# Kernel tuning notes

Measured on AMD Instinct MI355X. Metric: run time of the kernel, lower is better.

Reference implementation:

```python
import jax, jax.numpy as jnp
import numpy as np
import math

NTOKEN, NINP, NHID, SEQ, BATCH = 33278, 400, 1150, 70, 16
ODE_STEPS = 8  # fixed-step RK4 over t in [0,1] (reference for the adaptive solver)


def lstm_layer(x, h0, c0, Wih, Whh, bih, bhh):
    # x: [S, B, in]; PyTorch gate order i, f, g, o
    def step(carry, xt):
        h, c = carry
        g = xt @ Wih.T + h @ Whh.T + bih + bhh
        i, f, gg, o = jnp.split(g, 4, axis=-1)
        c = jax.nn.sigmoid(f) * c + jax.nn.sigmoid(i) * jnp.tanh(gg)
        h = jax.nn.sigmoid(o) * jnp.tanh(c)
        return (h, c), h
    (hT, cT), ys = jax.lax.scan(step, (h0, c0), x)
    return ys, hT, cT


def cnf_delta_logp(E, cnf_W, cnf_b):
    # ODEnet: f(t,z) = relu(Linear(concat([t, z]))); exact divergence since
    # Jacobian diag = relu'(pre) * diag(Wx). Integrates dz/dt=f, d(dlogp)/dt=-div f.
    wt = cnf_W[:, 0]
    Wx = cnf_W[:, 1:]
    dWx = jnp.diag(Wx)

    def f(t, z):
        pre = z @ Wx.T + t * wt + cnf_b          # [ntoken, ninp]
        div = jnp.sum((pre > 0) * dWx, axis=-1)  # exact trace of df/dz
        return jax.nn.relu(pre), -div

    dt = 1.0 / ODE_STEPS

    def rk4(carry, t):
        z, dl = carry
        k1z, k1l = f(t, z)
        k2z, k2l = f(t + dt / 2, z + dt / 2 * k1z)
        k3z, k3l = f(t + dt / 2, z + dt / 2 * k2z)
        k4z, k4l = f(t + dt, z + dt * k3z)
        z = z + dt / 6 * (k1z + 2 * k2z + 2 * k3z + k4z)
        dl = dl + dt / 6 * (k1l + 2 * k2l + 2 * k3l + k4l)
        return (z, dl), None

    ts = jnp.arange(ODE_STEPS, dtype=E.dtype) * dt
    (zT, dl), _ = jax.lax.scan(rk4, (E, jnp.zeros(E.shape[0], E.dtype)), ts)
    return dl  # [ntoken]


def setup_inputs() -> dict:
    key = jax.random.key(0)
    ks = jax.random.split(key, 16)
    s = 0.1
    inp = {
        "tokens": jax.random.randint(ks[0], (SEQ, BATCH), 0, NTOKEN),
        "h0_0": jnp.zeros((BATCH, NHID), jnp.float32),
        "c0_0": jnp.zeros((BATCH, NHID), jnp.float32),
        "h0_1": jnp.zeros((BATCH, NHID), jnp.float32),
        "c0_1": jnp.zeros((BATCH, NHID), jnp.float32),
        "h0_2": jnp.zeros((BATCH, NINP), jnp.float32),
        "c0_2": jnp.zeros((BATCH, NINP), jnp.float32),
        "emb_W": jax.random.uniform(ks[1], (NTOKEN, NINP), jnp.float32, -s, s),
        "Wih0": jax.random.normal(ks[2], (4 * NHID, NINP), jnp.float32) * 0.02,
        "Whh0": jax.random.normal(ks[3], (4 * NHID, NHID), jnp.float32) * 0.02,
        "bih0": jnp.zeros((4 * NHID,), jnp.float32),
        "bhh0": jnp.zeros((4 * NHID,), jnp.float32),
        "Wih1": jax.random.normal(ks[4], (4 * NHID, NHID), jnp.float32) * 0.02,
        "Whh1": jax.random.normal(ks[5], (4 * NHID, NHID), jnp.float32) * 0.02,
        "bih1": jnp.zeros((4 * NHID,), jnp.float32),
        "bhh1": jnp.zeros((4 * NHID,), jnp.float32),
        "Wih2": jax.random.normal(ks[6], (4 * NINP, NHID), jnp.float32) * 0.02,
        "Whh2": jax.random.normal(ks[7], (4 * NINP, NINP), jnp.float32) * 0.02,
        "bih2": jnp.zeros((4 * NINP,), jnp.float32),
        "bhh2": jnp.zeros((4 * NINP,), jnp.float32),
        "cnf_W": jax.random.normal(ks[8], (NINP, NINP + 1), jnp.float32) * 0.05,
        "cnf_b": jnp.zeros((NINP,), jnp.float32),
    }
    return inp


def reference(tokens, h0_0, c0_0, h0_1, c0_1, h0_2, c0_2, emb_W,
              Wih0, Whh0, bih0, bhh0, Wih1, Whh1, bih1, bhh1,
              Wih2, Whh2, bih2, bhh2, cnf_W, cnf_b):
    # embedding (eval mode: all dropouts are identity)
    x = emb_W[tokens]                               # [S, B, ninp]
    x, h1, c1 = lstm_layer(x, h0_0, c0_0, Wih0, Whh0, bih0, bhh0)
    x, h2, c2 = lstm_layer(x, h0_1, c0_1, Wih1, Whh1, bih1, bhh1)
    x, h3, c3 = lstm_layer(x, h0_2, c0_2, Wih2, Whh2, bih2, bhh2)
    # nhidlast == ninp -> no latent projection
    h = x.reshape(SEQ * BATCH, NINP)

    # MVNLogProb vectorized: -0.5 ||E_v - h_i||^2 - k/2 log(2*pi)
    e2 = jnp.sum(emb_W * emb_W, axis=-1)            # [ntoken]
    h2n = jnp.sum(h * h, axis=-1, keepdims=True)    # [SB, 1]
    sq = e2[None, :] - 2.0 * (h @ emb_W.T) + h2n    # [SB, ntoken]
    log_pz0 = -0.5 * sq - (NINP / 2.0) * math.log(2.0 * math.pi)

    # CNF delta_logp is identical for every token position (loop-invariant)
    delta = cnf_delta_logp(emb_W, cnf_W, cnf_b)     # [ntoken]
    log_pz1 = log_pz0 - delta[None, :]

    prob = jax.nn.softmax(log_pz1, axis=-1)
    log_prob = jnp.log(prob + 1e-8)
    model_output = log_prob.reshape(SEQ, BATCH, NTOKEN)
    return model_output, h1, c1, h2, c2, h3, c3
```

## Files before the change

kernel.cpp:

```cpp
#include <hip/hip_runtime.h>
#include <hip/hip_bf16.h>
#include <math.h>

#define SEQL 70
#define NTOK 33278
#define ODE_STEPS 8
#define NBLK 242
#define NGRP 16
#define CZS 418

typedef __attribute__((ext_vector_type(4))) float f32x4;
typedef __attribute__((ext_vector_type(8))) short s16x8;
typedef unsigned short u16;

__device__ __forceinline__ u16 f2b(float f) {
    union { float f; unsigned int u; } a; a.f = f;
    unsigned int u = a.u;
    return (u16)((u + 0x7FFFu + ((u >> 16) & 1u)) >> 16);
}
__device__ __forceinline__ float b2f(u16 s) {
    union { unsigned int u; float f; } a; a.u = ((unsigned int)s) << 16;
    return a.f;
}

__device__ __forceinline__ unsigned czoff(int row, int colb) {
    unsigned s = ((colb < 768 ? (row & 7) : (row & 3)) << 4);
    return (unsigned)(row * 832 + (colb ^ (int)s));
}

__global__ void cvt_pad_k(const float* __restrict__ src, u16* __restrict__ dst,
                          int G, int Nin, int Nop, int Kin, int Kp, int rs, int co) {
    size_t total = (size_t)G * Nop * Kp;
    for (size_t idx = (size_t)blockIdx.x * 256 + threadIdx.x; idx < total;
         idx += (size_t)gridDim.x * 256) {
        int k = (int)(idx % Kp);
        size_t t2 = idx / Kp;
        int j = (int)(t2 % Nop);
        int g = (int)(t2 / Nop);
        float v = 0.f;
        if (j < Nin && k < Kin) v = src[((size_t)g * Nin + j) * rs + co + k];
        dst[idx] = f2b(v);
    }
}

__global__ void bias_k(const float* __restrict__ bih, const float* __restrict__ bhh,
                       float* __restrict__ o, int Nin, int Nop) {
    int idx = blockIdx.x * 256 + threadIdx.x;
    if (idx >= 4 * Nop) return;
    int g = idx / Nop, j = idx % Nop;
    o[idx] = (j < Nin) ? (bih[g * Nin + j] + bhh[g * Nin + j]) : 0.f;
}

__global__ void wtdwx_k(const float* __restrict__ cw, float* __restrict__ wt,
                        float* __restrict__ dwx) {
    int i = blockIdx.x * 256 + threadIdx.x;
    if (i < 400) {
        wt[i]  = cw[(size_t)i * 401];
        dwx[i] = cw[(size_t)i * 401 + 1 + i];
    }
}

__global__ void h0cvt_k(const float* __restrict__ h0, u16* __restrict__ hb, int N, int Kp) {
    int idx = blockIdx.x * 256 + threadIdx.x;
    if (idx >= 16 * Kp) return;
    int b = idx / Kp, k = idx % Kp;
    hb[idx] = f2b(k < N ? h0[b * N + k] : 0.f);
}

__global__ void embed_k(const int* __restrict__ tok, const float* __restrict__ emb,
                        u16* __restrict__ x0) {
    int idx = blockIdx.x * 256 + threadIdx.x;
    if (idx >= 1152 * 416) return;
    int r = idx / 416, k = idx - r * 416;
    float v = 0.f;
    if (r < SEQL * 16 && k < 400) v = emb[(size_t)tok[r] * 400 + k];
    x0[idx] = f2b(v);
}

__global__ void rowsumsq_k(const float* __restrict__ X, float* __restrict__ o, int K) {
    int r = blockIdx.x;
    const float* xr = X + (size_t)r * K;
    int lane = threadIdx.x;
    float s = 0.f;
    for (int k = lane; k < K; k += 64) { float v = xr[k]; s += v * v; }
#pragma unroll
    for (int off = 1; off < 64; off <<= 1) s += __shfl_xor(s, off, 64);
    if (lane == 0) o[r] = s;
}

__global__ void ucomb_k(const float* __restrict__ e2, const float* __restrict__ dl,
                        float* __restrict__ u) {
    int i = blockIdx.x * 256 + threadIdx.x;
    if (i < NTOK) u[i] = -0.5f * e2[i] - dl[i];
}

__global__ void gemm_bt_k(const u16* __restrict__ A, const u16* __restrict__ B,
                          float* __restrict__ C, int Kp, int lda, int ldb, int ldc,
                          int Mreal, int Nreal, const float* __restrict__ uvec) {
    const int tid = threadIdx.x;
    const int wid = tid >> 6, lane = tid & 63;
    const int la = lane & 15, lk = (lane >> 4) * 8;
    const int m0 = blockIdx.y * 64 + wid * 16;
    const int n0 = blockIdx.x * 64;
    const f32x4 Z4 = {0.f, 0.f, 0.f, 0.f};
    f32x4 acc[4] = {Z4, Z4, Z4, Z4};
    const u16* Ar = A + (size_t)(m0 + la) * lda + lk;
    const u16* Br = B + (size_t)(n0 + la) * ldb + lk;
    for (int k = 0; k < Kp; k += 32) {
        s16x8 a = *(const s16x8*)(Ar + k);
#pragma unroll
        for (int nt = 0; nt < 4; ++nt) {
            s16x8 b = *(const s16x8*)(Br + (size_t)nt * 16 * ldb + k);
            acc[nt] = __builtin_amdgcn_mfma_f32_16x16x32_bf16(a, b, acc[nt], 0, 0, 0);
        }
    }
    const int mr = m0 + (lane >> 4) * 4;
#pragma unroll
    for (int nt = 0; nt < 4; ++nt) {
        int cc = n0 + nt * 16 + la;
        if (cc >= Nreal) continue;
        float uv = uvec ? uvec[cc] : 0.f;
#pragma unroll
        for (int r = 0; r < 4; ++r) {
            int rr = mr + r;
            if (rr < Mreal) C[(size_t)rr * ldc + cc] = acc[nt][r] + uv;
        }
    }
}

__device__ __forceinline__ void gridbar(int* base, int nb, int iter) {
    __syncthreads();
    if (threadIdx.x == 0) {
        int grp = blockIdx.x & (NGRP - 1);
        int gsz = nb / NGRP + ((grp < (nb % NGRP)) ? 1 : 0);
        int* gc   = base + grp * 16;
        int* root = base + 256;
        int* gen  = base + 272;
        int old = __hip_atomic_fetch_add(gc, 1, __ATOMIC_ACQ_REL, __HIP_MEMORY_SCOPE_AGENT);
        if ((old % gsz) == gsz - 1) {
            int r = __hip_atomic_fetch_add(root, 1, __ATOMIC_ACQ_REL, __HIP_MEMORY_SCOPE_AGENT);
            if ((r % NGRP) == NGRP - 1)
                __hip_atomic_fetch_add(gen, 1, __ATOMIC_ACQ_REL, __HIP_MEMORY_SCOPE_AGENT);
        }
        while (__hip_atomic_load(gen, __ATOMIC_RELAXED, __HIP_MEMORY_SCOPE_AGENT) <= iter)
            __builtin_amdgcn_s_sleep(8);
        (void)__hip_atomic_load(gen, __ATOMIC_ACQUIRE, __HIP_MEMORY_SCOPE_AGENT);
    }
    __syncthreads();
}

__global__ __launch_bounds__(768, 3) void lstm_k(
    const float* __restrict__ c00, const float* __restrict__ c01,
    const float* __restrict__ c02,
    const u16* __restrict__ Whh0p, const u16* __restrict__ Wih1p,
    const u16* __restrict__ Whh1p, const u16* __restrict__ Wih2p,
    const u16* __restrict__ Whh2p,
    const float* __restrict__ xW0, const float* __restrict__ bias2v,
    const float* __restrict__ bias1v,
    u16* __restrict__ ys0s, u16* __restrict__ ys1s, u16* __restrict__ ys2s,
    float* __restrict__ oh1, float* __restrict__ oc1,
    float* __restrict__ oh2, float* __restrict__ oc2,
    float* __restrict__ oh3, float* __restrict__ oc3,
    int* __restrict__ bar)
{
    __shared__ __align__(16) char smem[162816];
    u16* wlds = (u16*)smem;
    float* gl = (float*)(smem + 147456);
    const int tid = threadIdx.x;
    const int bid = blockIdx.x;
    const int wv = tid >> 6, lane = tid & 63;
    const int la = lane & 15, lg = lane >> 4;

    int role, jb;
    if (bid < 72) { role = 0; jb = bid; }
    else if (bid < 216) { role = 1; jb = bid - 72; }
    else { role = 2; jb = bid - 216; }

    if (role == 0) {
        for (int s = tid; s < 4 * 36 * 64; s += 768) {
            int ln = s & 63, kt = (s >> 6) % 36, nt = s / (36 * 64);
            int row = nt * 1152 + jb * 16 + (ln & 15);
            int col = kt * 32 + (ln >> 4) * 8;
            *(s16x8*)(wlds + (size_t)s * 8) =
                *(const s16x8*)(Whh0p + (size_t)row * 1152 + col);
        }
    } else if (role == 1) {
        for (int s = tid; s < 2 * 72 * 64; s += 768) {
            int ln = s & 63, kt = (s >> 6) % 72, nt = s / (72 * 64);
            int lr = nt * 16 + (ln & 15);
            int row = (lr >> 3) * 1152 + jb * 8 + (lr & 7);
            int col8 = (ln >> 4) * 8;
            const u16* src = (kt < 36)
                ? Wih1p + (size_t)row * 1152 + kt * 32 + col8
                : Whh1p + (size_t)row * 1152 + (kt - 36) * 32 + col8;
            *(s16x8*)(wlds + (size_t)s * 8) = *(const s16x8*)src;
        }
    }
    __syncthreads();

    float c_reg = 0.f;
    for (int sg = 0; sg < 72; ++sg) {
        int t = sg - role;
        if (t >= 0 && t < SEQL) {
            f32x4 acc = {0.f, 0.f, 0.f, 0.f};
            if (role == 0) {
                int nt = wv / 3, kg = wv - nt * 3;
                const u16* ar = ys0s + ((size_t)sg * 16 + la) * 1152 + lg * 8;
                for (int kt = kg * 12; kt < kg * 12 + 12; ++kt) {
                    s16x8 a = *(const s16x8*)(ar + kt * 32);
                    s16x8 b = *(const s16x8*)(wlds + ((size_t)(nt * 36 + kt) * 64 + lane) * 8);
                    acc = __builtin_amdgcn_mfma_f32_16x16x32_bf16(a, b, acc, 0, 0, 0);
                }
                *(f32x4*)(gl + wv * 320 + la * 20 + lg * 4) = acc;
            } else if (role == 1) {
                int nt = wv / 6, kg = wv - nt * 6;
                const u16* ax = ys0s + ((size_t)sg * 16 + la) * 1152 + lg * 8;
                const u16* ah = ys1s + ((size_t)(sg - 1) * 16 + la) * 1152 + lg * 8;
                for (int kt = kg * 12; kt < kg * 12 + 12; ++kt) {
                    s16x8 a = (kt < 36) ? *(const s16x8*)(ax + kt * 32)
                                        : *(const s16x8*)(ah + (kt - 36) * 32);
                    s16x8 b = *(const s16x8*)(wlds + ((size_t)(nt * 72 + kt) * 64 + lane) * 8);
                    acc = __builtin_amdgcn_mfma_f32_16x16x32_bf16(a, b, acc, 0, 0, 0);
                }
                *(f32x4*)(gl + wv * 320 + la * 20 + lg * 4) = acc;
            } else {
                int nt = wv / 3, kg = wv - nt * 3;
                int k0 = (kg * 49) / 3, k1 = ((kg + 1) * 49) / 3;
                const u16* ax = ys1s + ((size_t)(sg - 1) * 16 + la) * 1152 + lg * 8;
                const u16* ah = ys2s + ((size_t)(sg - 2) * 16 + la) * 416 + lg * 8;
                int wr = nt * 416 + jb * 16 + la;
                for (int kt = k0; kt < k1; ++kt) {
                    s16x8 a, b;
                    if (kt < 36) {
                        a = *(const s16x8*)(ax + kt * 32);
                        b = *(const s16x8*)(Wih2p + (size_t)wr * 1152 + kt * 32 + lg * 8);
                    } else {
                        a = *(const s16x8*)(ah + (kt - 36) * 32);
                        b = *(const s16x8*)(Whh2p + (size_t)wr * 416 + (kt - 36) * 32 + lg * 8);
                    }
                    acc = __builtin_amdgcn_mfma_f32_16x16x32_bf16(a, b, acc, 0, 0, 0);
                }
                *(f32x4*)(gl + wv * 320 + la * 20 + lg * 4) = acc;
            }
            __syncthreads();
            if (role == 1) {
                if (tid < 128) {
                    int u = tid & 7, tb = tid >> 3;
                    int ug = jb * 8 + u;
                    float gv[4];
#pragma unroll
                    for (int g = 0; g < 4; ++g) {
                        int lr = g * 8 + u;
                        int nt = lr >> 4, li = lr & 15;
                        float s = 0.f;
#pragma unroll
                        for (int kg = 0; kg < 6; ++kg)
                            s += gl[(nt * 6 + kg) * 320 + li * 20 + tb];
                        gv[g] = s + bias1v[g * 1152 + ug];
                    }
                    float cprev = (t == 0) ? ((ug < 1150) ? c01[tb * 1150 + ug] : 0.f) : c_reg;
                    float si = 1.f / (1.f + expf(-gv[0]));
                    float sf = 1.f / (1.f + expf(-gv[1]));
                    float so = 1.f / (1.f + expf(-gv[3]));
                    float cn = sf * cprev + si * tanhf(gv[2]);
                    float hn = so * tanhf(cn);
                    c_reg = cn;
                    if (ug < 1150) {
                        ys1s[((size_t)sg * 16 + tb) * 1152 + ug] = f2b(hn);
                        if (t == SEQL - 1) { oh2[tb * 1150 + ug] = hn; oc2[tb * 1150 + ug] = cn; }
                    }
                }
            } else if (tid < 256) {
                int u = tid & 15, tb = tid >> 4;
                int ug = jb * 16 + u;
                float gv[4];
#pragma unroll
                for (int g = 0; g < 4; ++g) {
                    float s = 0.f;
#pragma unroll
                    for (int kg = 0; kg < 3; ++kg)
                        s += gl[(g * 3 + kg) * 320 + u * 20 + tb];
                    gv[g] = s + ((role == 0)
                                 ? xW0[((size_t)t * 16 + tb) * 4608 + g * 1152 + ug]
                                 : bias2v[g * 416 + ug]);
                }
                int N = (role == 0) ? 1150 : 400;
                const float* c0i = (role == 0) ? c00 : c02;
                float cprev = (t == 0) ? ((ug < N) ? c0i[tb * N + ug] : 0.f) : c_reg;
                float si = 1.f / (1.f + expf(-gv[0]));
                float sf = 1.f / (1.f + expf(-gv[1]));
                float so = 1.f / (1.f + expf(-gv[3]));
                float cn = sf * cprev + si * tanhf(gv[2]);
                float hn = so * tanhf(cn);
                c_reg = cn;
                if (ug < N) {
                    if (role == 0) {
                        ys0s[((size_t)(sg + 1) * 16 + tb) * 1152 + ug] = f2b(hn);
                        if (t == SEQL - 1) { oh1[tb * 1150 + ug] = hn; oc1[tb * 1150 + ug] = cn; }
                    } else {
                        ys2s[((size_t)(sg - 1) * 16 + tb) * 416 + ug] = f2b(hn);
                        if (t == SEQL - 1) { oh3[tb * 400 + ug] = hn; oc3[tb * 400 + ug] = cn; }
                    }
                }
            }
        }
        gridbar(bar, NBLK, sg);
    }
}

__global__ __launch_bounds__(512, 2) void cnf_k(const float* __restrict__ emb,
                                                const u16* __restrict__ Wxp,
                                                const float* __restrict__ wt,
                                                const float* __restrict__ bv,
                                                const float* __restrict__ dwx,
                                                float* __restrict__ dl) {
    __shared__ float z0s[64 * CZS];
    __shared__ __align__(16) u16 zi[64 * 416];
    const int tid = threadIdx.x;
    const int m0 = blockIdx.x * 64;

    for (int idx = tid; idx < 64 * 416; idx += 512) {
        int r = idx / 416, cc = idx - r * 416;
        int row = m0 + r;
        float v = (cc < 400 && row < NTOK) ? emb[(size_t)row * 400 + cc] : 0.f;
        if (cc < 416) z0s[r * CZS + cc] = v;
        *(u16*)((char*)zi + czoff(r, cc * 2)) = f2b(v);
    }

    const int wv = tid >> 6, lane = tid & 63;
    const int la = lane & 15, lg = lane >> 4;
    const int lk = lg * 8;
    const int Qw = (wv == 0) ? 4 : 3;
    const int ntb = (wv == 0) ? 0 : 4 + (wv - 1) * 3;

    float wtq[4], bq[4], dwq[4];
#pragma unroll
    for (int q = 0; q < 4; ++q) {
        if (q < Qw) {
            int col = (ntb + q) * 16 + la;
            wtq[q] = wt[col]; bq[q] = bv[col]; dwq[q] = dwx[col];
        } else { wtq[q] = 0.f; bq[q] = 0.f; dwq[q] = 0.f; }
    }
    __syncthreads();

    const float dt = 1.f / ODE_STEPS;
    const f32x4 Z4 = {0.f, 0.f, 0.f, 0.f};
    float Aacc[4][4][4];
#pragma unroll
    for (int m = 0; m < 4; ++m)
#pragma unroll
        for (int q = 0; q < 4; ++q)
#pragma unroll
            for (int r = 0; r < 4; ++r) Aacc[m][q][r] = 0.f;
    float divp[4][4];
#pragma unroll
    for (int m = 0; m < 4; ++m)
#pragma unroll
        for (int r = 0; r < 4; ++r) divp[m][r] = 0.f;

#pragma unroll 1
    for (int st = 0; st < ODE_STEPS; ++st) {
        float t0 = st * dt;
#pragma unroll 1
        for (int s = 0; s < 4; ++s) {
            float ts = t0 + ((s == 0) ? 0.f : (s == 3) ? dt : 0.5f * dt);
            float wgt = (s == 1 || s == 2) ? 2.f : 1.f;
            float cs = (s == 2) ? dt : 0.5f * dt;
            f32x4 pre[4][4];
#pragma unroll
            for (int m = 0; m < 4; ++m)
#pragma unroll
                for (int q = 0; q < 4; ++q) pre[m][q] = Z4;
#pragma unroll 1
            for (int kk = 0; kk < 13; ++kk) {
                s16x8 b[4];
#pragma unroll
                for (int q = 0; q < 4; ++q)
                    if (q < Qw)
                        b[q] = *(const s16x8*)(Wxp + (size_t)((ntb + q) * 16 + la) * 416 +
                                               kk * 32 + lk);
#pragma unroll
                for (int m = 0; m < 4; ++m) {
                    int row = m * 16 + la;
                    s16x8 a = *(const s16x8*)((const char*)zi + czoff(row, (kk * 64 + lg * 16)));
#pragma unroll
                    for (int q = 0; q < 4; ++q)
                        if (q < Qw)
                            pre[m][q] = __builtin_amdgcn_mfma_f32_16x16x32_bf16(
                                a, b[q], pre[m][q], 0, 0, 0);
                }
            }
            __syncthreads();
#pragma unroll
            for (int m = 0; m < 4; ++m) {
#pragma unroll
                for (int q = 0; q < 4; ++q) {
                    if (q >= Qw) continue;
                    int col = (ntb + q) * 16 + la;
#pragma unroll
                    for (int r = 0; r < 4; ++r) {
                        int row = m * 16 + lg * 4 + r;
                        float pv = pre[m][q][r] + ts * wtq[q] + bq[q];
                        float kz = fmaxf(pv, 0.f);
                        if (pv > 0.f) divp[m][r] += dwq[q] * wgt;
                        float An = Aacc[m][q][r] + wgt * kz;
                        float ev;
                        if (s < 3) {
                            Aacc[m][q][r] = An;
                            ev = z0s[row * CZS + col] + cs * kz;
                        } else {
                            float zn = z0s[row * CZS + col] + (dt / 6.f) * An;
                            z0s[row * CZS + col] = zn;
                            Aacc[m][q][r] = 0.f;
                            ev = zn;
                        }
                        *(u16*)((char*)zi + czoff(row, col * 2)) = f2b(ev);
                    }
                }
            }
            __syncthreads();
        }
    }

#pragma unroll
    for (int m = 0; m < 4; ++m)
#pragma unroll
        for (int r = 0; r < 4; ++r) {
            float v = divp[m][r];
            v += __shfl_xor(v, 1, 64);
            v += __shfl_xor(v, 2, 64);
            v += __shfl_xor(v, 4, 64);
            v += __shfl_xor(v, 8, 64);
            divp[m][r] = v;
        }
    float* dsc = (float*)zi;
    if (la == 0) {
#pragma unroll
        for (int m = 0; m < 4; ++m)
#pragma unroll
            for (int r = 0; r < 4; ++r)
                dsc[wv * 64 + m * 16 + lg * 4 + r] = divp[m][r];
    }
    __syncthreads();
    for (int row = tid; row < 64; row += 512) {
        float s = 0.f;
#pragma unroll
        for (int w = 0; w < 8; ++w) s += dsc[w * 64 + row];
        if (m0 + row < NTOK) dl[m0 + row] = -(dt / 6.f) * s;
    }
}

__global__ void logsoftmax_k(float* __restrict__ L, int n) {
    const int row = blockIdx.x;
    float* R = L + (size_t)row * n;
    const int tid = threadIdx.x;
    float mx = -INFINITY, s = 0.f;
    for (int c = tid; c < n; c += 256) {
        float v = R[c];
        float nm = fmaxf(mx, v);
        s = s * expf(mx - nm) + expf(v - nm);
        mx = nm;
    }
#pragma unroll
    for (int off = 1; off < 64; off <<= 1) {
        float om = __shfl_xor(mx, off, 64);
        float os = __shfl_xor(s, off, 64);
        float nm = fmaxf(mx, om);
        s = s * expf(mx - nm) + os * expf(om - nm);
        mx = nm;
    }
    __shared__ float smx[4], ssm[4];
    if ((tid & 63) == 0) { smx[tid >> 6] = mx; ssm[tid >> 6] = s; }
    __syncthreads();
    float bm = fmaxf(fmaxf(smx[0], smx[1]), fmaxf(smx[2], smx[3]));
    float bs = ssm[0] * expf(smx[0] - bm) + ssm[1] * expf(smx[1] - bm) +
               ssm[2] * expf(smx[2] - bm) + ssm[3] * expf(smx[3] - bm);
    float lz = logf(bs);
    for (int c = tid; c < n; c += 256) {
        float v = R[c];
        R[c] = logf(expf(v - bm) + 1e-8f * bs) - lz;
    }
}

extern "C" void kernel_launch(void* const* d_in, const int* in_sizes, int n_in,
                              void* d_out, int out_size, void* d_ws, size_t ws_size,
                              hipStream_t stream) {
    const int*   tokens = (const int*)d_in[0];
    const float* h00 = (const float*)d_in[1];
    const float* c00 = (const float*)d_in[2];
    const float* h01 = (const float*)d_in[3];
    const float* c01 = (const float*)d_in[4];
    const float* h02 = (const float*)d_in[5];
    const float* c02 = (const float*)d_in[6];
    const float* embW = (const float*)d_in[7];
    const float* Wih0 = (const float*)d_in[8];
    const float* Whh0 = (const float*)d_in[9];
    const float* bih0 = (const float*)d_in[10];
    const float* bhh0 = (const float*)d_in[11];
    const float* Wih1 = (const float*)d_in[12];
    const float* Whh1 = (const float*)d_in[13];
    const float* bih1 = (const float*)d_in[14];
    const float* bhh1 = (const float*)d_in[15];
    const float* Wih2 = (const float*)d_in[16];
    const float* Whh2 = (const float*)d_in[17];
    const float* bih2 = (const float*)d_in[18];
    const float* bhh2 = (const float*)d_in[19];
    const float* cnfW = (const float*)d_in[20];
    const float* cnfb = (const float*)d_in[21];
    float* out = (float*)d_out;

    char* p = (char*)d_ws;
    auto alloc = [&](size_t bytes) -> void* {
        void* r = (void*)p;
        p += (bytes + 255) & ~(size_t)255;
        return r;
    };
    u16*   emb_p = (u16*)alloc((size_t)33280 * 416 * 2);
    u16*   x0    = (u16*)alloc((size_t)1152 * 416 * 2);
    u16*   ys0s  = (u16*)alloc((size_t)1136 * 1152 * 2);
    u16*   ys1s  = (u16*)alloc((size_t)1136 * 1152 * 2);
    u16*   ys2s  = (u16*)alloc((size_t)1184 * 416 * 2);
    float* xW    = (float*)alloc((size_t)1120 * 4608 * 4);
    u16*   Wih0p = (u16*)alloc((size_t)4608 * 416 * 2);
    u16*   Whh0p = (u16*)alloc((size_t)4608 * 1152 * 2);
    u16*   Wih1p = (u16*)alloc((size_t)4608 * 1152 * 2);
    u16*   Whh1p = (u16*)alloc((size_t)4608 * 1152 * 2);
    u16*   Wih2p = (u16*)alloc((size_t)1664 * 1152 * 2);
    u16*   Whh2p = (u16*)alloc((size_t)1664 * 416 * 2);
    float* bias0 = (float*)alloc((size_t)4608 * 4);
    float* bias1 = (float*)alloc((size_t)4608 * 4);
    float* bias2 = (float*)alloc((size_t)1664 * 4);
    u16*   Wxp   = (u16*)alloc((size_t)416 * 416 * 2);
    float* wtv   = (float*)alloc((size_t)400 * 4);
    float* dwx   = (float*)alloc((size_t)400 * 4);
    float* dl    = (float*)alloc((size_t)NTOK * 4);
    float* e2    = (float*)alloc((size_t)NTOK * 4);
    float* uvec  = (float*)alloc((size_t)NTOK * 4);
    int*   bar   = (int*)alloc(4096);

    size_t OM = (size_t)SEQL * 16 * NTOK;
    float* oh1 = out + OM;
    float* oc1 = oh1 + 16 * 1150;
    float* oh2 = oc1 + 16 * 1150;
    float* oc2 = oh2 + 16 * 1150;
    float* oh3 = oc2 + 16 * 1150;
    float* oc3 = oh3 + 16 * 400;

    hipMemsetAsync(bar, 0, 4096, stream);
    hipMemsetAsync(ys0s, 0, (size_t)1136 * 1152 * 2, stream);
    hipMemsetAsync(ys1s, 0, (size_t)1136 * 1152 * 2, stream);
    hipMemsetAsync(ys2s, 0, (size_t)1184 * 416 * 2, stream);

    cvt_pad_k<<<2048, 256, 0, stream>>>(Wih0, Wih0p, 4, 1150, 1152, 400, 416, 400, 0);
    cvt_pad_k<<<2048, 256, 0, stream>>>(Whh0, Whh0p, 4, 1150, 1152, 1150, 1152, 1150, 0);
    cvt_pad_k<<<2048, 256, 0, stream>>>(Wih1, Wih1p, 4, 1150, 1152, 1150, 1152, 1150, 0);
    cvt_pad_k<<<2048, 256, 0, stream>>>(Whh1, Whh1p, 4, 1150, 1152, 1150, 1152, 1150, 0);
    cvt_pad_k<<<2048, 256, 0, stream>>>(Wih2, Wih2p, 4, 400, 416, 1150, 1152, 1150, 0);
    cvt_pad_k<<<2048, 256, 0, stream>>>(Whh2, Whh2p, 4, 400, 416, 400, 416, 400, 0);
    cvt_pad_k<<<2048, 256, 0, stream>>>(embW, emb_p, 1, 33278, 33280, 400, 416, 400, 0);
    cvt_pad_k<<<2048, 256, 0, stream>>>(cnfW, Wxp, 1, 400, 416, 400, 416, 401, 1);
    bias_k<<<(4 * 1152 + 255) / 256, 256, 0, stream>>>(bih0, bhh0, bias0, 1150, 1152);
    bias_k<<<(4 * 1152 + 255) / 256, 256, 0, stream>>>(bih1, bhh1, bias1, 1150, 1152);
    bias_k<<<(4 * 416 + 255) / 256, 256, 0, stream>>>(bih2, bhh2, bias2, 400, 416);
    wtdwx_k<<<2, 256, 0, stream>>>(cnfW, wtv, dwx);
    rowsumsq_k<<<NTOK, 64, 0, stream>>>(embW, e2, 400);

    h0cvt_k<<<(16 * 1152 + 255) / 256, 256, 0, stream>>>(h00, ys0s, 1150, 1152);
    h0cvt_k<<<(16 * 1152 + 255) / 256, 256, 0, stream>>>(h01, ys1s, 1150, 1152);
    h0cvt_k<<<(16 * 416 + 255) / 256, 256, 0, stream>>>(h02, ys2s, 400, 416);

    cnf_k<<<520, 512, 0, stream>>>(embW, Wxp, wtv, cnfb, dwx, dl);
    ucomb_k<<<(NTOK + 255) / 256, 256, 0, stream>>>(e2, dl, uvec);

    embed_k<<<(1152 * 416 + 255) / 256, 256, 0, stream>>>(tokens, embW, x0);
    gemm_bt_k<<<dim3(72, 18), 256, 0, stream>>>(x0, Wih0p, xW, 416, 416, 416, 4608,
                                                1120, 4608, bias0);

    lstm_k<<<NBLK, 768, 0, stream>>>(
        c00, c01, c02, Whh0p, Wih1p, Whh1p, Wih2p, Whh2p,
        xW, bias2, bias1, ys0s, ys1s, ys2s,
        oh1, oc1, oh2, oc2, oh3, oc3, bar);

    gemm_bt_k<<<dim3(520, 18), 256, 0, stream>>>(ys2s + (size_t)16 * 416, emb_p, out,
                                                 416, 416, 416, NTOK, 1120, NTOK, uvec);
    logsoftmax_k<<<1120, 256, 0, stream>>>(out, NTOK);
}
```

Before: 2.998 ms.

## Replace global grid barrier with per-role barriers and restructure CNF kernel

The persistent LSTM kernel drops the single grid-wide barrier per skewed step. Each layer role now syncs only among its own blocks and waits on a generation counter published by the upstream layer. This lets layers run ahead as a dataflow pipeline instead of in lockstep. The CNF kernel also moves to 768 threads with 12 waves, swaps the MFMA operands so each lane holds 4 contiguous columns, and does vectorized z/weight loads and packed bf16 stores. The risks are correctness of the new barrier and counter layout, and higher register and LDS pressure in the CNF kernel.

```diff
diff --git a/kernel.cpp b/kernel.cpp
--- a/kernel.cpp
+++ b/kernel.cpp
@@ -6,8 +6,7 @@
 #define NTOK 33278
 #define ODE_STEPS 8
 #define NBLK 242
-#define NGRP 16
-#define CZS 418
+#define CZ4 404
 
 typedef __attribute__((ext_vector_type(4))) float f32x4;
 typedef __attribute__((ext_vector_type(8))) short s16x8;
@@ -128,22 +127,30 @@
     }
 }
 
-__device__ __forceinline__ void gridbar(int* base, int nb, int iter) {
+__device__ __forceinline__ void rolebar(int* base, int nb, int ngrp, int roleBlk, int iter) {
     __syncthreads();
     if (threadIdx.x == 0) {
-        int grp = blockIdx.x & (NGRP - 1);
-        int gsz = nb / NGRP + ((grp < (nb % NGRP)) ? 1 : 0);
+        int grp = roleBlk % ngrp;
+        int gsz = nb / ngrp + ((grp < (nb % ngrp)) ? 1 : 0);
         int* gc   = base + grp * 16;
-        int* root = base + 256;
-        int* gen  = base + 272;
+        int* root = base + ngrp * 16;
+        int* gen  = base + ngrp * 16 + 16;
         int old = __hip_atomic_fetch_add(gc, 1, __ATOMIC_ACQ_REL, __HIP_MEMORY_SCOPE_AGENT);
         if ((old % gsz) == gsz - 1) {
             int r = __hip_atomic_fetch_add(root, 1, __ATOMIC_ACQ_REL, __HIP_MEMORY_SCOPE_AGENT);
-            if ((r % NGRP) == NGRP - 1)
+            if ((r % ngrp) == ngrp - 1)
                 __hip_atomic_fetch_add(gen, 1, __ATOMIC_ACQ_REL, __HIP_MEMORY_SCOPE_AGENT);
         }
         while (__hip_atomic_load(gen, __ATOMIC_RELAXED, __HIP_MEMORY_SCOPE_AGENT) <= iter)
-            __builtin_amdgcn_s_sleep(8);
+            __builtin_amdgcn_s_sleep(4);
+        (void)__hip_atomic_load(gen, __ATOMIC_ACQUIRE, __HIP_MEMORY_SCOPE_AGENT);
+    }
+    __syncthreads();
+}
+__device__ __forceinline__ void waitgen(int* gen, int needed) {
+    if (threadIdx.x == 0) {
+        while (__hip_atomic_load(gen, __ATOMIC_RELAXED, __HIP_MEMORY_SCOPE_AGENT) < needed)
+            __builtin_amdgcn_s_sleep(4);
         (void)__hip_atomic_load(gen, __ATOMIC_ACQUIRE, __HIP_MEMORY_SCOPE_AGENT);
     }
     __syncthreads();
@@ -176,6 +183,12 @@
     else if (bid < 216) { role = 1; jb = bid - 72; }
     else { role = 2; jb = bid - 216; }
 
+    int* bar0 = bar;
+    int* bar1 = bar + 256;
+    int* bar2 = bar + 768;
+    int* g0 = bar0 + 144;
+    int* g1 = bar1 + 272;
+
     if (role == 0) {
         for (int s = tid; s < 4 * 36 * 64; s += 768) {
             int ln = s & 63, kt = (s >> 6) % 36, nt = s / (36 * 64);
@@ -199,164 +212,163 @@
     __syncthreads();
 
     float c_reg = 0.f;
-    for (int sg = 0; sg < 72; ++sg) {
-        int t = sg - role;
-        if (t >= 0 && t < SEQL) {
-            f32x4 acc = {0.f, 0.f, 0.f, 0.f};
-            if (role == 0) {
-                int nt = wv / 3, kg = wv - nt * 3;
-                const u16* ar = ys0s + ((size_t)sg * 16 + la) * 1152 + lg * 8;
-                for (int kt = kg * 12; kt < kg * 12 + 12; ++kt) {
-                    s16x8 a = *(const s16x8*)(ar + kt * 32);
-                    s16x8 b = *(const s16x8*)(wlds + ((size_t)(nt * 36 + kt) * 64 + lane) * 8);
-                    acc = __builtin_amdgcn_mfma_f32_16x16x32_bf16(a, b, acc, 0, 0, 0);
+    for (int t = 0; t < SEQL; ++t) {
+        if (role == 1) waitgen(g0, t + 1);
+        else if (role == 2) waitgen(g1, t + 1);
+
+        f32x4 acc = {0.f, 0.f, 0.f, 0.f};
+        if (role == 0) {
+            int nt = wv / 3, kg = wv - nt * 3;
+            const u16* ar = ys0s + ((size_t)t * 16 + la) * 1152 + lg * 8;
+            for (int kt = kg * 12; kt < kg * 12 + 12; ++kt) {
+                s16x8 a = *(const s16x8*)(ar + kt * 32);
+                s16x8 b = *(const s16x8*)(wlds + ((size_t)(nt * 36 + kt) * 64 + lane) * 8);
+                acc = __builtin_amdgcn_mfma_f32_16x16x32_bf16(a, b, acc, 0, 0, 0);
+            }
+            *(f32x4*)(gl + wv * 320 + la * 20 + lg * 4) = acc;
+        } else if (role == 1) {
+            int nt = wv / 6, kg = wv - nt * 6;
+            const u16* ax = ys0s + ((size_t)(t + 1) * 16 + la) * 1152 + lg * 8;
+            const u16* ah = ys1s + ((size_t)t * 16 + la) * 1152 + lg * 8;
+            for (int kt = kg * 12; kt < kg * 12 + 12; ++kt) {
+                s16x8 a = (kt < 36) ? *(const s16x8*)(ax + kt * 32)
+                                    : *(const s16x8*)(ah + (kt - 36) * 32);
+                s16x8 b = *(const s16x8*)(wlds + ((size_t)(nt * 72 + kt) * 64 + lane) * 8);
+                acc = __builtin_amdgcn_mfma_f32_16x16x32_bf16(a, b, acc, 0, 0, 0);
+            }
+            *(f32x4*)(gl + wv * 320 + la * 20 + lg * 4) = acc;
+        } else {
+            int nt = wv / 3, kg = wv - nt * 3;
+            int k0 = (kg * 49) / 3, k1 = ((kg + 1) * 49) / 3;
+            const u16* ax = ys1s + ((size_t)(t + 1) * 16 + la) * 1152 + lg * 8;
+            const u16* ah = ys2s + ((size_t)t * 16 + la) * 416 + lg * 8;
+            int wr = nt * 416 + jb * 16 + la;
+            for (int kt = k0; kt < k1; ++kt) {
+                s16x8 a, b;
+                if (kt < 36) {
+                    a = *(const s16x8*)(ax + kt * 32);
+                    b = *(const s16x8*)(Wih2p + (size_t)wr * 1152 + kt * 32 + lg * 8);
+                } else {
+                    a = *(const s16x8*)(ah + (kt - 36) * 32);
+                    b = *(const s16x8*)(Whh2p + (size_t)wr * 416 + (kt - 36) * 32 + lg * 8);
                 }
-                *(f32x4*)(gl + wv * 320 + la * 20 + lg * 4) = acc;
-            } else if (role == 1) {
-                int nt = wv / 6, kg = wv - nt * 6;
-                const u16* ax = ys0s + ((size_t)sg * 16 + la) * 1152 + lg * 8;
-                const u16* ah = ys1s + ((size_t)(sg - 1) * 16 + la) * 1152 + lg * 8;
-                for (int kt = kg * 12; kt < kg * 12 + 12; ++kt) {
-                    s16x8 a = (kt < 36) ? *(const s16x8*)(ax + kt * 32)
-                                        : *(const s16x8*)(ah + (kt - 36) * 32);
-                    s16x8 b = *(const s16x8*)(wlds + ((size_t)(nt * 72 + kt) * 64 + lane) * 8);
-                    acc = __builtin_amdgcn_mfma_f32_16x16x32_bf16(a, b, acc, 0, 0, 0);
+                acc = __builtin_amdgcn_mfma_f32_16x16x32_bf16(a, b, acc, 0, 0, 0);
+            }
+            *(f32x4*)(gl + wv * 320 + la * 20 + lg * 4) = acc;
+        }
+        __syncthreads();
+        if (role == 1) {
+            if (tid < 128) {
+                int u = tid & 7, tb = tid >> 3;
+                int ug = jb * 8 + u;
+                float gv[4];
+#pragma unroll
+                for (int g = 0; g < 4; ++g) {
+                    int lr = g * 8 + u;
+                    int nt = lr >> 4, li = lr & 15;
+                    float s = 0.f;
+#pragma unroll
+                    for (int kg = 0; kg < 6; ++kg)
+                        s += gl[(nt * 6 + kg) * 320 + li * 20 + tb];
+                    gv[g] = s + bias1v[g * 1152 + ug];
                 }
-                *(f32x4*)(gl + wv * 320 + la * 20 + lg * 4) = acc;
-            } else {
-                int nt = wv / 3, kg = wv - nt * 3;
-                int k0 = (kg * 49) / 3, k1 = ((kg + 1) * 49) / 3;
-                const u16* ax = ys1s + ((size_t)(sg - 1) * 16 + la) * 1152 + lg * 8;
-                const u16* ah = ys2s + ((size_t)(sg - 2) * 16 + la) * 416 + lg * 8;
-                int wr = nt * 416 + jb * 16 + la;
-                for (int kt = k0; kt < k1; ++kt) {
-                    s16x8 a, b;
-                    if (kt < 36) {
-                        a = *(const s16x8*)(ax + kt * 32);
-                        b = *(const s16x8*)(Wih2p + (size_t)wr * 1152 + kt * 32 + lg * 8);
-                    } else {
-                        a = *(const s16x8*)(ah + (kt - 36) * 32);
-                        b = *(const s16x8*)(Whh2p + (size_t)wr * 416 + (kt - 36) * 32 + lg * 8);
-                    }
-                    acc = __builtin_amdgcn_mfma_f32_16x16x32_bf16(a, b, acc, 0, 0, 0);
-                }
-                *(f32x4*)(gl + wv * 320 + la * 20 + lg * 4) = acc;
-            }
-            __syncthreads();
-            if (role == 1) {
-                if (tid < 128) {
-                    int u = tid & 7, tb = tid >> 3;
-                    int ug = jb * 8 + u;
-                    float gv[4];
-#pragma unroll
-                    for (int g = 0; g < 4; ++g) {
-                        int lr = g * 8 + u;
-                        int nt = lr >> 4, li = lr & 15;
-                        float s = 0.f;
-#pragma unroll
-                        for (int kg = 0; kg < 6; ++kg)
-                            s += gl[(nt * 6 + kg) * 320 + li * 20 + tb];
-                        gv[g] = s + bias1v[g * 1152 + ug];
-                    }
-                    float cprev = (t == 0) ? ((ug < 1150) ? c01[tb * 1150 + ug] : 0.f) : c_reg;
-                    float si = 1.f / (1.f + expf(-gv[0]));
-                    float sf = 1.f / (1.f + expf(-gv[1]));
-                    float so = 1.f / (1.f + expf(-gv[3]));
-                    float cn = sf * cprev + si * tanhf(gv[2]);
-                    float hn = so * tanhf(cn);
-                    c_reg = cn;
-                    if (ug < 1150) {
-                        ys1s[((size_t)sg * 16 + tb) * 1152 + ug] = f2b(hn);
-                        if (t == SEQL - 1) { oh2[tb * 1150 + ug] = hn; oc2[tb * 1150 + ug] = cn; }
-                    }
-                }
-            } else if (tid < 256) {
-                int u = tid & 15, tb = tid >> 4;
-                int ug = jb * 16 + u;
-                float gv[4];
-#pragma unroll
-                for (int g = 0; g < 4; ++g) {
-                    float s = 0.f;
-#pragma unroll
-                    for (int kg = 0; kg < 3; ++kg)
-                        s += gl[(g * 3 + kg) * 320 + u * 20 + tb];
-                    gv[g] = s + ((role == 0)
-                                 ? xW0[((size_t)t * 16 + tb) * 4608 + g * 1152 + ug]
-                                 : bias2v[g * 416 + ug]);
-                }
-                int N = (role == 0) ? 1150 : 400;
-                const float* c0i = (role == 0) ? c00 : c02;
-                float cprev = (t == 0) ? ((ug < N) ? c0i[tb * N + ug] : 0.f) : c_reg;
+                float cprev = (t == 0) ? ((ug < 1150) ? c01[tb * 1150 + ug] : 0.f) : c_reg;
                 float si = 1.f / (1.f + expf(-gv[0]));
                 float sf = 1.f / (1.f + expf(-gv[1]));
                 float so = 1.f / (1.f + expf(-gv[3]));
                 float cn = sf * cprev + si * tanhf(gv[2]);
                 float hn = so * tanhf(cn);
                 c_reg = cn;
-                if (ug < N) {
-                    if (role == 0) {
-                        ys0s[((size_t)(sg + 1) * 16 + tb) * 1152 + ug] = f2b(hn);
-                        if (t == SEQL - 1) { oh1[tb * 1150 + ug] = hn; oc1[tb * 1150 + ug] = cn; }
-                    } else {
-                        ys2s[((size_t)(sg - 1) * 16 + tb) * 416 + ug] = f2b(hn);
-                        if (t == SEQL - 1) { oh3[tb * 400 + ug] = hn; oc3[tb * 400 + ug] = cn; }
-                    }
+                if (ug < 1150) {
+                    ys1s[((size_t)(t + 1) * 16 + tb) * 1152 + ug] = f2b(hn);
+                    if (t == SEQL - 1) { oh2[tb * 1150 + ug] = hn; oc2[tb * 1150 + ug] = cn; }
                 }
             }
-        }
-        gridbar(bar, NBLK, sg);
-    }
-}
-
-__global__ __launch_bounds__(512, 2) void cnf_k(const float* __restrict__ emb,
+        } else if (tid < 256) {
+            int u = tid & 15, tb = tid >> 4;
+            int ug = jb * 16 + u;
+            float gv[4];
+#pragma unroll
+            for (int g = 0; g < 4; ++g) {
+                float s = 0.f;
+#pragma unroll
+                for (int kg = 0; kg < 3; ++kg)
+                    s += gl[(g * 3 + kg) * 320 + u * 20 + tb];
+                gv[g] = s + ((role == 0)
+                             ? xW0[((size_t)t * 16 + tb) * 4608 + g * 1152 + ug]
+                             : bias2v[g * 416 + ug]);
+            }
+            int N = (role == 0) ? 1150 : 400;
+            const float* c0i = (role == 0) ? c00 : c02;
+            float cprev = (t == 0) ? ((ug < N) ? c0i[tb * N + ug] : 0.f) : c_reg;
+            float si = 1.f / (1.f + expf(-gv[0]));
+            float sf = 1.f / (1.f + expf(-gv[1]));
+            float so = 1.f / (1.f + expf(-gv[3]));
+            float cn = sf * cprev + si * tanhf(gv[2]);
+            float hn = so * tanhf(cn);
+            c_reg = cn;
+            if (ug < N) {
+                if (role == 0) {
+                    ys0s[((size_t)(t + 1) * 16 + tb) * 1152 + ug] = f2b(hn);
+                    if (t == SEQL - 1) { oh1[tb * 1150 + ug] = hn; oc1[tb * 1150 + ug] = cn; }
+                } else {
+                    ys2s[((size_t)(t + 1) * 16 + tb) * 416 + ug] = f2b(hn);
+                    if (t == SEQL - 1) { oh3[tb * 400 + ug] = hn; oc3[tb * 400 + ug] = cn; }
+                }
+            }
+        }
+        if (role == 0) rolebar(bar0, 72, 8, jb, t);
+        else if (role == 1) rolebar(bar1, 144, 16, jb, t);
+        else rolebar(bar2, 26, 1, jb, t);
+    }
+}
+
+__global__ __launch_bounds__(768, 3) void cnf_k(const float* __restrict__ emb,
                                                 const u16* __restrict__ Wxp,
-                                                const float* __restrict__ wt,
-                                                const float* __restrict__ bv,
-                                                const float* __restrict__ dwx,
+                                                const float* __restrict__ wtv,
+                                                const float* __restrict__ bvv,
+                                                const float* __restrict__ dwxv,
                                                 float* __restrict__ dl) {
-    __shared__ float z0s[64 * CZS];
-    __shared__ __align__(16) u16 zi[64 * 416];
+    __shared__ __align__(16) char smem[159744];
+    float* z0s = (float*)smem;
+    char*  zib = smem + 64 * CZ4 * 4;
+    float* dsc = (float*)(smem + 64 * CZ4 * 4 + 64 * 832);
     const int tid = threadIdx.x;
     const int m0 = blockIdx.x * 64;
-
-    for (int idx = tid; idx < 64 * 416; idx += 512) {
+    const int wv = tid >> 6, lane = tid & 63;
+    const int la = lane & 15, lg = lane >> 4;
+
+    for (int idx = tid; idx < 64 * 416; idx += 768) {
         int r = idx / 416, cc = idx - r * 416;
         int row = m0 + r;
         float v = (cc < 400 && row < NTOK) ? emb[(size_t)row * 400 + cc] : 0.f;
-        if (cc < 416) z0s[r * CZS + cc] = v;
-        *(u16*)((char*)zi + czoff(r, cc * 2)) = f2b(v);
-    }
-
-    const int wv = tid >> 6, lane = tid & 63;
-    const int la = lane & 15, lg = lane >> 4;
-    const int lk = lg * 8;
-    const int Qw = (wv == 0) ? 4 : 3;
-    const int ntb = (wv == 0) ? 0 : 4 + (wv - 1) * 3;
-
-    float wtq[4], bq[4], dwq[4];
-#pragma unroll
-    for (int q = 0; q < 4; ++q) {
+        if (cc < 400) z0s[r * CZ4 + cc] = v;
+        *(u16*)(zib + czoff(r, cc * 2)) = f2b(v);
+    }
+
+    const int Qw = (wv == 0) ? 3 : 2;
+    const int ntb = (wv == 0) ? 0 : 3 + 2 * (wv - 1);
+    const f32x4 Z4 = {0.f, 0.f, 0.f, 0.f};
+    f32x4 wt4[3], bv4[3], dw4[3];
+#pragma unroll
+    for (int q = 0; q < 3; ++q) {
+        wt4[q] = Z4; bv4[q] = Z4; dw4[q] = Z4;
         if (q < Qw) {
-            int col = (ntb + q) * 16 + la;
-            wtq[q] = wt[col]; bq[q] = bv[col]; dwq[q] = dwx[col];
-        } else { wtq[q] = 0.f; bq[q] = 0.f; dwq[q] = 0.f; }
-    }
-    __syncthreads();
-
-    const float dt = 1.f / ODE_STEPS;
-    const f32x4 Z4 = {0.f, 0.f, 0.f, 0.f};
-    float Aacc[4][4][4];
+            int c4 = (ntb + q) * 16 + lg * 4;
+            wt4[q] = *(const f32x4*)(wtv + c4);
+            bv4[q] = *(const f32x4*)(bvv + c4);
+            dw4[q] = *(const f32x4*)(dwxv + c4);
+        }
+    }
+    __syncthreads();
+
+    const float dt = 1.f / ODE_STEPS, dt6 = dt / 6.f;
+    f32x4 Aacc[4][3];
 #pragma unroll
     for (int m = 0; m < 4; ++m)
 #pragma unroll
-        for (int q = 0; q < 4; ++q)
-#pragma unroll
-            for (int r = 0; r < 4; ++r) Aacc[m][q][r] = 0.f;
-    float divp[4][4];
-#pragma unroll
-    for (int m = 0; m < 4; ++m)
-#pragma unroll
-        for (int r = 0; r < 4; ++r) divp[m][r] = 0.f;
+        for (int q = 0; q < 3; ++q) Aacc[m][q] = Z4;
+    float divacc[4] = {0.f, 0.f, 0.f, 0.f};
 
 #pragma unroll 1
     for (int st = 0; st < ODE_STEPS; ++st) {
@@ -366,87 +378,79 @@
             float ts = t0 + ((s == 0) ? 0.f : (s == 3) ? dt : 0.5f * dt);
             float wgt = (s == 1 || s == 2) ? 2.f : 1.f;
             float cs = (s == 2) ? dt : 0.5f * dt;
-            f32x4 pre[4][4];
+            f32x4 pre[4][3];
 #pragma unroll
             for (int m = 0; m < 4; ++m)
 #pragma unroll
-                for (int q = 0; q < 4; ++q) pre[m][q] = Z4;
-#pragma unroll 1
+                for (int q = 0; q < 3; ++q) pre[m][q] = Z4;
             for (int kk = 0; kk < 13; ++kk) {
-                s16x8 b[4];
-#pragma unroll
-                for (int q = 0; q < 4; ++q)
+                s16x8 aW[3];
+#pragma unroll
+                for (int q = 0; q < 3; ++q)
                     if (q < Qw)
-                        b[q] = *(const s16x8*)(Wxp + (size_t)((ntb + q) * 16 + la) * 416 +
-                                               kk * 32 + lk);
+                        aW[q] = *(const s16x8*)(Wxp + (size_t)((ntb + q) * 16 + la) * 416 +
+                                                kk * 32 + lg * 8);
 #pragma unroll
                 for (int m = 0; m < 4; ++m) {
-                    int row = m * 16 + la;
-                    s16x8 a = *(const s16x8*)((const char*)zi + czoff(row, (kk * 64 + lg * 16)));
-#pragma unroll
-                    for (int q = 0; q < 4; ++q)
+                    int rr = m * 16 + la;
+                    s16x8 bz = *(const s16x8*)(zib + czoff(rr, (kk * 32 + lg * 8) * 2));
+#pragma unroll
+                    for (int q = 0; q < 3; ++q)
                         if (q < Qw)
                             pre[m][q] = __builtin_amdgcn_mfma_f32_16x16x32_bf16(
-                                a, b[q], pre[m][q], 0, 0, 0);
+                                aW[q], bz, pre[m][q], 0, 0, 0);
                 }
             }
             __syncthreads();
+            f32x4 tb4[3], dwg[3];
+#pragma unroll
+            for (int q = 0; q < 3; ++q)
+                if (q < Qw) { tb4[q] = ts * wt4[q] + bv4[q]; dwg[q] = wgt * dw4[q]; }
 #pragma unroll
             for (int m = 0; m < 4; ++m) {
-#pragma unroll
-                for (int q = 0; q < 4; ++q) {
+                int row = m * 16 + la;
+#pragma unroll
+                for (int q = 0; q < 3; ++q) {
                     if (q >= Qw) continue;
-                    int col = (ntb + q) * 16 + la;
+                    int c4 = (ntb + q) * 16 + lg * 4;
+                    f32x4 z04 = *(const f32x4*)(z0s + row * CZ4 + c4);
+                    f32x4 ev;
 #pragma unroll
                     for (int r = 0; r < 4; ++r) {
-                        int row = m * 16 + lg * 4 + r;
-                        float pv = pre[m][q][r] + ts * wtq[q] + bq[q];
+                        float pv = pre[m][q][r] + tb4[q][r];
                         float kz = fmaxf(pv, 0.f);
-                        if (pv > 0.f) divp[m][r] += dwq[q] * wgt;
-                        float An = Aacc[m][q][r] + wgt * kz;
-                        float ev;
+                        if (pv > 0.f) divacc[m] += dwg[q][r];
                         if (s < 3) {
-                            Aacc[m][q][r] = An;
-                            ev = z0s[row * CZS + col] + cs * kz;
+                            Aacc[m][q][r] += wgt * kz;
+                            ev[r] = z04[r] + cs * kz;
                         } else {
-                            float zn = z0s[row * CZS + col] + (dt / 6.f) * An;
-                            z0s[row * CZS + col] = zn;
-                            Aacc[m][q][r] = 0.f;
-                            ev = zn;
+                            float zn = z04[r] + dt6 * (Aacc[m][q][r] + kz);
+                            ev[r] = zn; z04[r] = zn; Aacc[m][q][r] = 0.f;
                         }
-                        *(u16*)((char*)zi + czoff(row, col * 2)) = f2b(ev);
                     }
+                    if (s == 3) *(f32x4*)(z0s + row * CZ4 + c4) = z04;
+                    ushort4 pk;
+                    pk.x = f2b(ev[0]); pk.y = f2b(ev[1]);
+                    pk.z = f2b(ev[2]); pk.w = f2b(ev[3]);
+                    *(ushort4*)(zib + czoff(row, c4 * 2)) = pk;
                 }
             }
             __syncthreads();
         }
     }
-
-#pragma unroll
-    for (int m = 0; m < 4; ++m)
-#pragma unroll
-        for (int r = 0; r < 4; ++r) {
-            float v = divp[m][r];
-            v += __shfl_xor(v, 1, 64);
-            v += __shfl_xor(v, 2, 64);
-            v += __shfl_xor(v, 4, 64);
-            v += __shfl_xor(v, 8, 64);
-            divp[m][r] = v;
-        }
-    float* dsc = (float*)zi;
-    if (la == 0) {
-#pragma unroll
-        for (int m = 0; m < 4; ++m)
-#pragma unroll
-            for (int r = 0; r < 4; ++r)
-                dsc[wv * 64 + m * 16 + lg * 4 + r] = divp[m][r];
-    }
-    __syncthreads();
-    for (int row = tid; row < 64; row += 512) {
+#pragma unroll
+    for (int m = 0; m < 4; ++m) {
+        float v = divacc[m];
+        v += __shfl_xor(v, 16, 64);
+        v += __shfl_xor(v, 32, 64);
+        if (lane < 16) dsc[wv * 64 + m * 16 + la] = v;
+    }
+    __syncthreads();
+    for (int row = tid; row < 64; row += 768) {
         float s = 0.f;
 #pragma unroll
-        for (int w = 0; w < 8; ++w) s += dsc[w * 64 + row];
-        if (m0 + row < NTOK) dl[m0 + row] = -(dt / 6.f) * s;
+        for (int w = 0; w < 12; ++w) s += dsc[w * 64 + row];
+        if (m0 + row < NTOK) dl[m0 + row] = -dt6 * s;
     }
 }
 
@@ -569,7 +573,7 @@
     h0cvt_k<<<(16 * 1152 + 255) / 256, 256, 0, stream>>>(h01, ys1s, 1150, 1152);
     h0cvt_k<<<(16 * 416 + 255) / 256, 256, 0, stream>>>(h02, ys2s, 400, 416);
 
-    cnf_k<<<520, 512, 0, stream>>>(embW, Wxp, wtv, cnfb, dwx, dl);
+    cnf_k<<<520, 768, 0, stream>>>(embW, Wxp, wtv, cnfb, dwx, dl);
     ucomb_k<<<(NTOK + 255) / 256, 256, 0, stream>>>(e2, dl, uvec);
 
     embed_k<<<(1152 * 416 + 255) / 256, 256, 0, stream>>>(tokens, embW, x0);
```

Result: slower. 5.785 ms (+92.9%).
